# Performance work log

Measured on AMD Instinct MI355X. Metric: run time of the kernel, lower is better.

## Reference

```python
import jax, jax.numpy as jnp
import numpy as np

LN_EPS = 1e-5
BN_EPS = 1e-5


def setup_inputs() -> dict:
    key = jax.random.key(0)
    k0, k1, k2, k3 = jax.random.split(key, 4)
    N, C, T, V, S = 128, 64, 128, 25, 3  # batch, channels, frames, joints, subsets
    rel = C // 8                          # rel_channels = 8
    inner = rel * S                       # hidden_dim * n_heads = 24
    x = jax.random.normal(k0, (N, C, T, V), dtype=jnp.float32)
    # graph adjacency parameter (3 subsets over 25 joints); small positive values
    PA = jax.random.uniform(k1, (S, V, V), dtype=jnp.float32) * 0.1
    ln_gamma = jnp.ones((C,), jnp.float32)
    ln_beta = jnp.zeros((C,), jnp.float32)
    # to_qk: Linear(C, 2*inner), weight init normal(0, 1) per source
    Wqk = jax.random.normal(k2, (2 * inner, C), dtype=jnp.float32)
    bqk = jnp.zeros((2 * inner,), jnp.float32)
    # conv_branch_init: normal(0, sqrt(2/(out*1*1*branches)))
    conv_w = jax.random.normal(k3, (S, C, C), dtype=jnp.float32) * np.float32(np.sqrt(2.0 / (C * S)))
    conv_b = jnp.zeros((S, C), jnp.float32)
    bn_gamma = jnp.ones((C,), jnp.float32)
    bn_beta = jnp.zeros((C,), jnp.float32)
    bn_mean = jnp.zeros((C,), jnp.float32)
    bn_var = jnp.ones((C,), jnp.float32)
    return {"x": x, "PA": PA, "ln_gamma": ln_gamma, "ln_beta": ln_beta,
            "Wqk": Wqk, "bqk": bqk, "conv_w": conv_w, "conv_b": conv_b,
            "bn_gamma": bn_gamma, "bn_beta": bn_beta, "bn_mean": bn_mean, "bn_var": bn_var}


def reference(x, PA, ln_gamma, ln_beta, Wqk, bqk, conv_w, conv_b,
              bn_gamma, bn_beta, bn_mean, bn_var):
    N, C, T, V = x.shape
    S = PA.shape[0]                       # num_subset == n_heads
    rel = Wqk.shape[0] // (2 * S)         # hidden dim per head
    scale = rel ** (-0.5)

    xv = jnp.transpose(x, (0, 2, 3, 1))   # n t v c

    # --- SelfAttention: LayerNorm -> Linear -> per-head softmax(q k^T) ---
    mu = jnp.mean(xv, axis=-1, keepdims=True)
    var = jnp.mean(jnp.square(xv - mu), axis=-1, keepdims=True)
    yn = (xv - mu) * jax.lax.rsqrt(var + LN_EPS) * ln_gamma + ln_beta
    qk = yn @ Wqk.T + bqk                 # n t v (2*inner)
    inner = qk.shape[-1] // 2
    q = qk[..., :inner].reshape(N, T, V, S, rel)
    k = qk[..., inner:].reshape(N, T, V, S, rel)
    dots = jnp.einsum('ntihd,ntjhd->nthij', q, k) * scale  # (n,t,h,V,V)
    attn = jax.nn.softmax(dots, axis=-1)

    # --- attention-modulated adjacency + per-subset aggregation ---
    A = attn * PA[None, None]             # (n,t,h,V,V)
    z = jnp.einsum('nthij,ntjc->nthic', A, xv)  # (n,t,h,V,C) messages per subset
    # per-subset 1x1 conv then sum over subsets
    out = jnp.einsum('nthvc,hoc->notv', z, conv_w) \
        + jnp.sum(conv_b, axis=0)[None, :, None, None]  # (n,C,t,V)

    # --- BatchNorm2d (eval-mode with provided stats) + residual + ReLU ---
    bn_out = (out - bn_mean[None, :, None, None]) \
        * jax.lax.rsqrt(bn_var + BN_EPS)[None, :, None, None] \
        * bn_gamma[None, :, None, None] + bn_beta[None, :, None, None]
    return jax.nn.relu(bn_out + x)        # down is identity since in_c == out_c
```

## Files before the change

kernel.cpp:

```cpp
#include <hip/hip_runtime.h>
#include <hip/hip_bf16.h>
#include <math.h>

typedef __attribute__((ext_vector_type(8))) short bf16x8;
typedef __attribute__((ext_vector_type(4))) float f32x4;

__device__ inline unsigned short f2bf(float f) {
    return __builtin_bit_cast(unsigned short, __float2bfloat16(f));
}
__device__ inline float bf2f(unsigned short u) {
    return __bfloat162float(__builtin_bit_cast(__hip_bfloat16, u));
}
__device__ inline bf16x8 cvt8(float4 a, float4 b) {
    bf16x8 r;
    r[0]=(short)f2bf(a.x); r[1]=(short)f2bf(a.y); r[2]=(short)f2bf(a.z); r[3]=(short)f2bf(a.w);
    r[4]=(short)f2bf(b.x); r[5]=(short)f2bf(b.y); r[6]=(short)f2bf(b.z); r[7]=(short)f2bf(b.w);
    return r;
}
__device__ inline void split8(float4 a, float4 b, bf16x8& hi, bf16x8& lo) {
    float f[8] = {a.x,a.y,a.z,a.w,b.x,b.y,b.z,b.w};
    #pragma unroll
    for (int i = 0; i < 8; ++i) {
        unsigned short h = f2bf(f[i]);
        hi[i] = (short)h;
        lo[i] = (short)f2bf(f[i] - bf2f(h));
    }
}

#define LDS_FLOATS 6403

__global__ __launch_bounds__(256, 6)
void agcn_fused_kernel(const float* __restrict__ x,
                       const float* __restrict__ PA,
                       const float* __restrict__ ln_g, const float* __restrict__ ln_b,
                       const float* __restrict__ Wqk, const float* __restrict__ bqk,
                       const float* __restrict__ conv_w, const float* __restrict__ conv_b,
                       const float* __restrict__ bn_g, const float* __restrict__ bn_b,
                       const float* __restrict__ bn_m, const float* __restrict__ bn_v,
                       float* __restrict__ out)
{
    __shared__ float lds[LDS_FLOATS];
    float* xv = lds;
    unsigned short* ynh = (unsigned short*)(lds + 1628);
    unsigned short* ynl = (unsigned short*)(lds + 2428);
    unsigned short* A_bf = (unsigned short*)(lds + 1628);
    float* qkb  = lds + 3228;
    unsigned short* xvT = (unsigned short*)(lds + 3228);
    float* Abuf = lds + 4528;
    unsigned short* zA  = (unsigned short*)(lds + 1628);
    float* res  = lds + 4528;

    const int bid = blockIdx.x;
    const int sid = ((bid & 7) << 11) | (bid >> 3);
    const int n = sid >> 7, t = sid & 127;
    const int tid = threadIdx.x;
    const int lane = tid & 63, w = tid >> 6;
    const int g = lane >> 4, l15 = lane & 15;

    const int o = 16 * w + l15;
    float4 cw_f[12];
    #pragma unroll
    for (int kt = 0; kt < 6; ++kt) {
        const float* wp = &conv_w[(kt >> 1) * 4096 + o * 64 + (kt & 1) * 32 + 8 * g];
        cw_f[2*kt]   = *(const float4*)wp;
        cw_f[2*kt+1] = *(const float4*)(wp + 4);
    }
    float4 wq_f[4];
    float bq = 0.f;
    if (w < 3) {
        const int j = 16 * w + l15;
        #pragma unroll
        for (int ks = 0; ks < 2; ++ks) {
            const float* wp = &Wqk[j * 64 + ks * 32 + 8 * g];
            wq_f[2*ks]   = *(const float4*)wp;
            wq_f[2*ks+1] = *(const float4*)(wp + 4);
        }
        bq = bqk[j];
    }

    const float* xbase = x + (size_t)n * 204800 + t * 25;
    for (int idx = tid; idx < 1600; idx += 256) {
        int c = idx / 25, v = idx - c * 25;
        xv[v * 65 + c] = xbase[c * 3200 + v];
    }

    bf16x8 cw[6];
    #pragma unroll
    for (int kt = 0; kt < 6; ++kt) cw[kt] = cvt8(cw_f[2*kt], cw_f[2*kt+1]);
    bf16x8 wqh[2], wql[2];
    if (w < 3) {
        #pragma unroll
        for (int ks = 0; ks < 2; ++ks) split8(wq_f[2*ks], wq_f[2*ks+1], wqh[ks], wql[ks]);
    }
    __syncthreads();

    {
        float lg = ln_g[lane], lb = ln_b[lane];
        for (int v = w; v < 25; v += 4) {
            float val = xv[v * 65 + lane];
            float s = val;
            for (int off = 32; off; off >>= 1) s += __shfl_xor(s, off);
            float mu = s * (1.0f / 64.0f);
            float d = val - mu;
            float s2 = d * d;
            for (int off = 32; off; off >>= 1) s2 += __shfl_xor(s2, off);
            float rstd = rsqrtf(s2 * (1.0f / 64.0f) + 1e-5f);
            float y = d * rstd * lg + lb;
            unsigned short h = f2bf(y);
            unsigned short l = f2bf(y - bf2f(h));
            int idx = (v * 64 + lane) ^ ((v & 7) << 3);
            ynh[idx] = h;
            ynl[idx] = l;
        }
    }
    __syncthreads();

    if (w < 3) {
        const int j = 16 * w + l15;
        #pragma unroll
        for (int mt = 0; mt < 2; ++mt) {
            f32x4 acc = {bq, bq, bq, bq};
            #pragma unroll
            for (int ks = 0; ks < 2; ++ks) {
                int row = 16 * mt + l15;
                int idx = (row * 64 + ks * 32 + 8 * g) ^ ((row & 7) << 3);
                bf16x8 ah = *(bf16x8*)&ynh[idx];
                bf16x8 al = *(bf16x8*)&ynl[idx];
                acc = __builtin_amdgcn_mfma_f32_16x16x32_bf16(al, wqh[ks], acc, 0, 0, 0);
                acc = __builtin_amdgcn_mfma_f32_16x16x32_bf16(ah, wql[ks], acc, 0, 0, 0);
                acc = __builtin_amdgcn_mfma_f32_16x16x32_bf16(ah, wqh[ks], acc, 0, 0, 0);
            }
            #pragma unroll
            for (int reg = 0; reg < 4; ++reg) {
                int v = 16 * mt + 4 * g + reg;
                if (v < 25) qkb[v * 52 + j] = acc[reg];
            }
        }
    }
    __syncthreads();

    for (int idx = tid; idx < 1875; idx += 256) {
        int h = idx / 625, r = idx - h * 625;
        int i = r / 25, j = r - i * 25;
        const float4* q = (const float4*)&qkb[i * 52 + h * 8];
        const float4* k = (const float4*)&qkb[j * 52 + 24 + h * 8];
        float4 q0 = q[0], q1 = q[1], k0 = k[0], k1 = k[1];
        float d = q0.x*k0.x + q0.y*k0.y + q0.z*k0.z + q0.w*k0.w
                + q1.x*k1.x + q1.y*k1.y + q1.z*k1.z + q1.w*k1.w;
        Abuf[idx] = d * 0.35355339059327373f;
    }
    __syncthreads();

    if (tid < 75) {
        int h = tid / 25, i = tid - h * 25;
        const float* row = &Abuf[h * 625 + i * 25];
        const float* pa = &PA[h * 625 + i * 25];
        float m = row[0];
        #pragma unroll
        for (int j = 1; j < 25; ++j) m = fmaxf(m, row[j]);
        float e[25];
        float s = 0.f;
        #pragma unroll
        for (int j = 0; j < 25; ++j) { e[j] = __expf(row[j] - m); s += e[j]; }
        float inv = 1.0f / s;
        unsigned short* ar = &A_bf[(h * 25 + i) * 40];
        #pragma unroll
        for (int j = 0; j < 25; ++j) ar[j] = f2bf(e[j] * inv * pa[j]);
        #pragma unroll
        for (int j = 25; j < 32; ++j) ar[j] = 0;
    }
    for (int idx = tid; idx < 2560; idx += 256) {
        int c = idx / 40, j = idx - c * 40;
        float val = (j < 25) ? xv[j * 65 + c] : 0.f;
        xvT[idx] = f2bf(val);
    }
    __syncthreads();

    f32x4 zacc[5];
    {
        bf16x8 bfrag = *(bf16x8*)&xvT[(16 * w + l15) * 40 + 8 * g];
        #pragma unroll
        for (int mt = 0; mt < 5; ++mt) {
            bf16x8 afrag = *(bf16x8*)&A_bf[(16 * mt + l15) * 40 + 8 * g];
            f32x4 a = {0.f, 0.f, 0.f, 0.f};
            zacc[mt] = __builtin_amdgcn_mfma_f32_16x16x32_bf16(afrag, bfrag, a, 0, 0, 0);
        }
    }
    __syncthreads();

    #pragma unroll
    for (int mt = 0; mt < 5; ++mt) {
        #pragma unroll
        for (int reg = 0; reg < 4; ++reg) {
            int r = 16 * mt + 4 * g + reg;
            if (r < 75) {
                int h = r / 25, i = r - h * 25;
                zA[i * 200 + h * 64 + 16 * w + l15] = f2bf(zacc[mt][reg]);
            }
        }
    }
    __syncthreads();

    {
        float bg = bn_g[o], bv = bn_v[o], bb = bn_b[o], bm = bn_m[o];
        float cb = conv_b[o] + conv_b[64 + o] + conv_b[128 + o];

        const int r1 = (16 + l15 < 25) ? (16 + l15) : 0;
        f32x4 acc0 = {0.f, 0.f, 0.f, 0.f}, acc1 = {0.f, 0.f, 0.f, 0.f};
        #pragma unroll
        for (int kt = 0; kt < 6; ++kt) {
            bf16x8 a0 = *(bf16x8*)&zA[l15 * 200 + 32 * kt + 8 * g];
            bf16x8 a1 = *(bf16x8*)&zA[r1 * 200 + 32 * kt + 8 * g];
            acc0 = __builtin_amdgcn_mfma_f32_16x16x32_bf16(a0, cw[kt], acc0, 0, 0, 0);
            acc1 = __builtin_amdgcn_mfma_f32_16x16x32_bf16(a1, cw[kt], acc1, 0, 0, 0);
        }
        float sc = bg * rsqrtf(bv + 1e-5f);
        float bi = cb * sc + bb - bm * sc;
        #pragma unroll
        for (int reg = 0; reg < 4; ++reg) {
            int v = 4 * g + reg;
            float val = acc0[reg] * sc + bi + xv[v * 65 + o];
            res[o * 25 + v] = fmaxf(val, 0.f);
        }
        #pragma unroll
        for (int reg = 0; reg < 4; ++reg) {
            int v = 16 + 4 * g + reg;
            if (v < 25) {
                float val = acc1[reg] * sc + bi + xv[v * 65 + o];
                res[o * 25 + v] = fmaxf(val, 0.f);
            }
        }
    }
    __syncthreads();

    {
        float* ob = out + (size_t)n * 204800 + t * 25;
        for (int idx = tid; idx < 1600; idx += 256) {
            int c = idx / 25, v = idx - c * 25;
            ob[c * 3200 + v] = res[idx];
        }
    }
}

extern "C" void kernel_launch(void* const* d_in, const int* in_sizes, int n_in,
                              void* d_out, int out_size, void* d_ws, size_t ws_size,
                              hipStream_t stream) {
    const float* x      = (const float*)d_in[0];
    const float* PA     = (const float*)d_in[1];
    const float* ln_g   = (const float*)d_in[2];
    const float* ln_b   = (const float*)d_in[3];
    const float* Wqk    = (const float*)d_in[4];
    const float* bqk    = (const float*)d_in[5];
    const float* conv_w = (const float*)d_in[6];
    const float* conv_b = (const float*)d_in[7];
    const float* bn_g   = (const float*)d_in[8];
    const float* bn_b   = (const float*)d_in[9];
    const float* bn_m   = (const float*)d_in[10];
    const float* bn_v   = (const float*)d_in[11];
    float* outp = (float*)d_out;

    agcn_fused_kernel<<<dim3(128 * 128), dim3(256), 0, stream>>>(
        x, PA, ln_g, ln_b, Wqk, bqk, conv_w, conv_b,
        bn_g, bn_b, bn_m, bn_v, outp);
}
```

Baseline: 248.0 us.

## Vectorize LayerNorm across 8 lanes per joint and drop block swizzle

LayerNorm now gives each joint 8 lanes, each handling 8 channels. This replaces one wavefront per joint with two 6-step shuffle reductions per row, and writes the hi/lo bf16 outputs with 128-bit LDS stores. Variance switches to the single-pass E[x^2]-mu^2 form, which is slightly less numerically robust. The block-index swizzle that interleaved batches across blocks is also removed, so blocks now map linearly to (n,t), which may change cache and memory locality.

```diff
diff --git a/kernel.cpp b/kernel.cpp
--- a/kernel.cpp
+++ b/kernel.cpp
@@ -51,8 +51,7 @@
     float* res  = lds + 4528;
 
     const int bid = blockIdx.x;
-    const int sid = ((bid & 7) << 11) | (bid >> 3);
-    const int n = sid >> 7, t = sid & 127;
+    const int n = bid >> 7, t = bid & 127;
     const int tid = threadIdx.x;
     const int lane = tid & 63, w = tid >> 6;
     const int g = lane >> 4, l15 = lane & 15;
@@ -77,6 +76,11 @@
         }
         bq = bqk[j];
     }
+    const int c0 = (lane & 7) << 3;
+    const float4 lg0 = *(const float4*)&ln_g[c0];
+    const float4 lg1 = *(const float4*)&ln_g[c0 + 4];
+    const float4 lb0 = *(const float4*)&ln_b[c0];
+    const float4 lb1 = *(const float4*)&ln_b[c0 + 4];
 
     const float* xbase = x + (size_t)n * 204800 + t * 25;
     for (int idx = tid; idx < 1600; idx += 256) {
@@ -95,22 +99,33 @@
     __syncthreads();
 
     {
-        float lg = ln_g[lane], lb = ln_b[lane];
-        for (int v = w; v < 25; v += 4) {
-            float val = xv[v * 65 + lane];
-            float s = val;
-            for (int off = 32; off; off >>= 1) s += __shfl_xor(s, off);
-            float mu = s * (1.0f / 64.0f);
-            float d = val - mu;
-            float s2 = d * d;
-            for (int off = 32; off; off >>= 1) s2 += __shfl_xor(s2, off);
-            float rstd = rsqrtf(s2 * (1.0f / 64.0f) + 1e-5f);
-            float y = d * rstd * lg + lb;
-            unsigned short h = f2bf(y);
-            unsigned short l = f2bf(y - bf2f(h));
-            int idx = (v * 64 + lane) ^ ((v & 7) << 3);
-            ynh[idx] = h;
-            ynl[idx] = l;
+        const int vr = (w << 3) + (lane >> 3);
+        if (vr < 25) {
+            float xa[8];
+            #pragma unroll
+            for (int i = 0; i < 8; ++i) xa[i] = xv[vr * 65 + c0 + i];
+            float s1 = ((xa[0]+xa[1])+(xa[2]+xa[3])) + ((xa[4]+xa[5])+(xa[6]+xa[7]));
+            float s2 = ((xa[0]*xa[0]+xa[1]*xa[1])+(xa[2]*xa[2]+xa[3]*xa[3]))
+                     + ((xa[4]*xa[4]+xa[5]*xa[5])+(xa[6]*xa[6]+xa[7]*xa[7]));
+            s1 += __shfl_xor(s1, 1);  s2 += __shfl_xor(s2, 1);
+            s1 += __shfl_xor(s1, 2);  s2 += __shfl_xor(s2, 2);
+            s1 += __shfl_xor(s1, 4);  s2 += __shfl_xor(s2, 4);
+            float mu = s1 * (1.0f / 64.0f);
+            float var = s2 * (1.0f / 64.0f) - mu * mu;
+            float rstd = rsqrtf(var + 1e-5f);
+            float lg[8] = {lg0.x,lg0.y,lg0.z,lg0.w,lg1.x,lg1.y,lg1.z,lg1.w};
+            float lb[8] = {lb0.x,lb0.y,lb0.z,lb0.w,lb1.x,lb1.y,lb1.z,lb1.w};
+            bf16x8 hh8, ll8;
+            #pragma unroll
+            for (int i = 0; i < 8; ++i) {
+                float y = (xa[i] - mu) * rstd * lg[i] + lb[i];
+                unsigned short hh = f2bf(y);
+                hh8[i] = (short)hh;
+                ll8[i] = (short)f2bf(y - bf2f(hh));
+            }
+            int base = (vr * 64 + c0) ^ ((vr & 7) << 3);
+            *(bf16x8*)&ynh[base] = hh8;
+            *(bf16x8*)&ynl[base] = ll8;
         }
     }
     __syncthreads();
```

Measured after the change: 297.4 us. +20.0%, slower.
